# Performance work log

Measured on AMD Instinct MI355X. Metric: run time of the kernel, lower is better.

## Reference

```python
import jax, jax.numpy as jnp
import numpy as np

SEQ_LEN = 4096
EMBED = 1024
HIDDEN = 128
BATCH = 8


def setup_inputs() -> dict:
    key = jax.random.key(0)
    k_in, k_q, k_k, k_v = jax.random.split(key, 4)
    inputs = jax.random.normal(k_in, (BATCH, SEQ_LEN, EMBED), dtype=jnp.float32)
    # nn.Linear(embed, hidden, bias=False) weights; stored [hidden, embed] in torch,
    # we keep [embed, hidden] for x @ W.
    scale = 1.0 / np.sqrt(EMBED)
    Wq = jax.random.uniform(k_q, (EMBED, HIDDEN), jnp.float32, -scale, scale)
    Wk = jax.random.uniform(k_k, (EMBED, HIDDEN), jnp.float32, -scale, scale)
    Wv = jax.random.uniform(k_v, (EMBED, HIDDEN), jnp.float32, -scale, scale)
    return {"inputs": inputs, "Wq": Wq, "Wk": Wk, "Wv": Wv}


def reference(inputs, Wq, Wk, Wv):
    # Single-head causal scaled dot-product attention.
    q = jnp.einsum("bse,eh->bsh", inputs, Wq)
    k = jnp.einsum("bse,eh->bsh", inputs, Wk)
    v = jnp.einsum("bse,eh->bsh", inputs, Wv)
    d_k = q.shape[-1]
    q = q / jnp.sqrt(jnp.asarray(d_k, q.dtype))
    scores = jnp.einsum("bqh,bkh->bqk", q, k)  # [B, S, S]
    seq = scores.shape[-1]
    causal = jnp.tril(jnp.ones((seq, seq), dtype=bool))
    scores = jnp.where(causal, scores, jnp.asarray(-jnp.inf, scores.dtype))
    weights = jax.nn.softmax(scores, axis=-1)
    return jnp.einsum("bqk,bkh->bqh", weights, v)
```

## Files before the change

### kernel.cpp

```cpp
#include <hip/hip_runtime.h>
#include <stdint.h>

#define B_ 8
#define S_ 4096
#define E_ 1024
#define H_ 128
#define M_ (B_*S_)

typedef __attribute__((ext_vector_type(8))) short short8;
typedef __attribute__((ext_vector_type(4))) float f32x4;
typedef __attribute__((ext_vector_type(16))) float f32x16;

static constexpr float QSCALE = 0.08838834764831845f;

__device__ __forceinline__ unsigned short f2bf(float f) {
    uint32_t u = __float_as_uint(f);
    u += 0x7fffu + ((u >> 16) & 1u);
    return (unsigned short)(u >> 16);
}

__device__ __forceinline__ uint32_t cvt_pk_bf16(float a, float b) {
    uint32_t r;
    asm("v_cvt_pk_bf16_f32 %0, %1, %2" : "=v"(r) : "v"(a), "v"(b));
    return r;
}

__device__ __forceinline__ float bf2f(uint32_t u) {
    return __uint_as_float(u << 16);
}

__device__ __forceinline__ void gl16(const void* g, void* s) {
    __builtin_amdgcn_global_load_lds(
        (const __attribute__((address_space(1))) unsigned int*)g,
        (__attribute__((address_space(3))) unsigned int*)s, 16, 0, 0);
}

__global__ __launch_bounds__(256)
void prep_w_kernel(const float* __restrict__ Wq, const float* __restrict__ Wk,
                   const float* __restrict__ Wv, unsigned short* __restrict__ Wt)
{
    int id = blockIdx.x*256 + threadIdx.x;
    int which = id >> 14;
    int rem = id & 16383;
    int h = rem >> 7, kc = rem & 127;
    const float* __restrict__ W = (which==0)?Wq:((which==1)?Wk:Wv);
    const float scale = (which==0)? QSCALE : 1.0f;
    uint32_t u[4];
    #pragma unroll
    for (int p=0;p<4;++p) {
        unsigned short a = f2bf(W[(size_t)(kc*8 + 2*p  )*H_ + h] * scale);
        unsigned short b = f2bf(W[(size_t)(kc*8 + 2*p+1)*H_ + h] * scale);
        u[p] = (uint32_t)a | ((uint32_t)b << 16);
    }
    uint4 v; v.x=u[0]; v.y=u[1]; v.z=u[2]; v.w=u[3];
    int gp = (kc >> 3)*128 + (((kc & 7) ^ (h & 7)) << 4);
    *(uint4*)((unsigned char*)Wt + (size_t)(which*H_ + h)*2048 + gp) = v;
}

__device__ __forceinline__ void proj_stage(unsigned char* buf,
                                           const unsigned char* xb,
                                           const unsigned char* Wb,
                                           int i, int w, int l)
{
    #pragma unroll
    for (int j=0;j<8;++j) {
        int cb = (j*8 + w) * 1024;
        int A  = cb + (l << 4);
        if (cb < 16384) {
            int sub = A >> 13;
            int A2  = A & 8191;
            int row = A2 >> 7, col = A2 & 127;
            gl16(xb + (size_t)row*4096 + i*256 + sub*128 + (col ^ ((row & 7) << 4)),
                 buf + cb);
        } else {
            int A2 = A - 16384;
            int wr = A2 >> 7, wc = A2 & 127;
            gl16(Wb + (size_t)wr*2048 + i*128 + wc, buf + cb);
        }
    }
}

__global__ __launch_bounds__(512)
void proj_kernel(const float* __restrict__ x, const unsigned short* __restrict__ Wt,
                 unsigned short* __restrict__ Qg, unsigned short* __restrict__ Kg,
                 unsigned short* __restrict__ Vtg)
{
    const int t = threadIdx.x;
    const int w = t >> 6, l = t & 63;
    const int grp = l >> 4, li = l & 15;
    const int rg = w & 1, cg = w >> 1;
    const int rb = blockIdx.x;
    const int row0 = rb * 64;

    __shared__ __align__(128) unsigned char smem[65536];
    unsigned short* epi = (unsigned short*)smem;

    const unsigned char* xb = (const unsigned char*)x + (size_t)row0*4096;
    const unsigned char* Wb = (const unsigned char*)Wt;

    f32x4 acc[2][6];
    const f32x4 zz = {0.f,0.f,0.f,0.f};
    #pragma unroll
    for (int mt=0;mt<2;++mt)
        #pragma unroll
        for (int nt=0;nt<6;++nt) acc[mt][nt] = zz;

    proj_stage(smem, xb, Wb, 0, w, l);
    __syncthreads();

    for (int i=0; i<16; ++i) {
        const unsigned char* sX = smem;
        const unsigned char* sW = smem + 16384;

        #pragma unroll
        for (int ks=0;ks<2;++ks) {
            short8 af[2];
            #pragma unroll
            for (int mt=0;mt<2;++mt) {
                int row = rg*32 + mt*16 + li;
                int sw = (row & 7) << 4;
                float4 a0 = *(const float4*)(sX + ks*8192 + row*128 + ((grp*32     ) ^ sw));
                float4 a1 = *(const float4*)(sX + ks*8192 + row*128 + ((grp*32 + 16) ^ sw));
                union { uint32_t u[4]; short8 s; } pa;
                pa.u[0] = cvt_pk_bf16(a0.x, a0.y);
                pa.u[1] = cvt_pk_bf16(a0.z, a0.w);
                pa.u[2] = cvt_pk_bf16(a1.x, a1.y);
                pa.u[3] = cvt_pk_bf16(a1.z, a1.w);
                af[mt] = pa.s;
            }
            #pragma unroll
            for (int nt=0;nt<6;++nt) {
                int wr = cg*96 + nt*16 + li;
                short8 bf = *(const short8*)(sW + wr*128 + ((ks*64 + grp*16) ^ ((wr & 7) << 4)));
                acc[0][nt] = __builtin_amdgcn_mfma_f32_16x16x32_bf16(af[0], bf, acc[0][nt], 0,0,0);
                acc[1][nt] = __builtin_amdgcn_mfma_f32_16x16x32_bf16(af[1], bf, acc[1][nt], 0,0,0);
            }
        }

        __syncthreads();
        if (i+1 < 16) {
            proj_stage(smem, xb, Wb, i+1, w, l);
            __syncthreads();
        }
    }

    const int bidx = rb >> 6;
    const int srow = (rb & 63) * 64;

    if (cg < 2) {
        #pragma unroll
        for (int mt=0;mt<2;++mt)
            #pragma unroll
            for (int nt=0;nt<6;++nt)
                #pragma unroll
                for (int r=0;r<4;++r) {
                    int rowl = rg*32 + mt*16 + grp*4 + r;
                    int col  = cg*96 + nt*16 + li;
                    epi[rowl*208 + col] = f2bf(acc[mt][nt][r]);
                }
    }
    __syncthreads();
    #pragma unroll
    for (int i=0;i<2;++i) {
        int idx = i*512 + t;
        int row = idx >> 4, cc = idx & 15;
        uint4 v = *(const uint4*)((const unsigned char*)epi + row*416 + cc*16);
        *(uint4*)((unsigned char*)Qg + (size_t)(row0+row)*256 + cc*16) = v;
    }
    {
        int row = t >> 3, cc = t & 7;
        uint4 v = *(const uint4*)((const unsigned char*)epi + row*416 + 256 + cc*16);
        *(uint4*)((unsigned char*)Kg + (size_t)(row0+row)*256 + cc*16) = v;
    }
    __syncthreads();

    if (cg >= 2) {
        #pragma unroll
        for (int mt=0;mt<2;++mt)
            #pragma unroll
            for (int nt=0;nt<6;++nt)
                #pragma unroll
                for (int r=0;r<4;++r) {
                    int rowl = rg*32 + mt*16 + grp*4 + r;
                    int col  = (cg-2)*96 + nt*16 + li;
                    epi[rowl*208 + col] = f2bf(acc[mt][nt][r]);
                }
    }
    __syncthreads();
    {
        int row = t >> 3, cc = t & 7;
        uint4 v = *(const uint4*)((const unsigned char*)epi + row*416 + cc*16);
        *(uint4*)((unsigned char*)Kg + (size_t)(row0+row)*256 + 128 + cc*16) = v;
    }
    #pragma unroll
    for (int i=0;i<2;++i) {
        int idx = i*512 + t;
        int h = idx >> 3, sc = idx & 7;
        uint32_t u[4];
        #pragma unroll
        for (int p=0;p<4;++p) {
            unsigned short a = epi[(sc*8 + 2*p    )*208 + 64 + h];
            unsigned short b = epi[(sc*8 + 2*p + 1)*208 + 64 + h];
            u[p] = (uint32_t)a | ((uint32_t)b << 16);
        }
        uint4 v; v.x=u[0]; v.y=u[1]; v.z=u[2]; v.w=u[3];
        *(uint4*)(Vtg + (size_t)(bidx*H_ + h)*S_ + srow + sc*8) = v;
    }
}

__device__ __forceinline__ void stage_tile(unsigned char* buf,
                                           const unsigned char* Kb,
                                           const unsigned char* Vb,
                                           int kt, int w, int l)
{
    unsigned char* sVb = buf + 16384;
    #pragma unroll
    for (int j=0;j<2;++j) {
        int A = w*2048 + j*1024 + (l<<4);
        int krow = A >> 8;
        int kin  = A & 255;
        gl16(Kb + (size_t)kt*16384 + krow*256 + (kin ^ ((krow&7)<<4)),
             buf + w*2048 + j*1024);
        int h   = A >> 7;
        int vin = A & 127;
        gl16(Vb + (size_t)h*8192 + (size_t)kt*128 + (vin ^ ((h&7)<<4)),
             sVb + w*2048 + j*1024);
    }
}

__global__ __launch_bounds__(512, 2)
void attn_p1(const unsigned short* __restrict__ Qg,
             const unsigned short* __restrict__ Kg,
             const unsigned short* __restrict__ Vtg,
             unsigned short* __restrict__ Pp, float* __restrict__ Ml)
{
    const int t    = threadIdx.x;
    const int w    = t >> 6;
    const int l    = t & 63;
    const int hi   = l >> 5;
    const int c31  = l & 31;
    const int gid  = blockIdx.x;
    const int b    = gid & 7;
    const int rr   = gid >> 3;
    const int c4   = rr & 3;
    const int pr   = rr >> 2;

    __shared__ __align__(128) unsigned char smem[65536];

    const size_t bbase = (size_t)b * S_ * H_;
    const unsigned char* Kb = (const unsigned char*)(Kg + bbase);
    const unsigned char* Vb = (const unsigned char*)(Vtg + (size_t)b*H_*S_);
    const int swzq = (c31 & 7) << 4;

    int cur = 0;
    for (int ph = 0; ph < 2; ++ph) {
        const int qt   = ph ? (15 - pr) : pr;
        const int q0   = qt * 256;
        const int qw0  = q0 + w*32;
        const int qrow = qw0 + c31;
        const int nkt  = 4*(qt+1);

        short8 qf[8];
        {
            const unsigned short* qp = Qg + bbase + (size_t)qrow * H_;
            #pragma unroll
            for (int ks=0; ks<8; ++ks)
                qf[ks] = *(const short8*)(qp + ks*16 + hi*8);
        }

        f32x16 oacc[4];
        #pragma unroll
        for (int ht=0; ht<4; ++ht)
            #pragma unroll
            for (int r=0; r<16; ++r) oacc[ht][r] = 0.f;
        float mrun = -1e30f, lrun = 0.f;

        stage_tile(smem + cur*32768, Kb, Vb, c4, w, l);
        __syncthreads();

        for (int kt = c4; kt < nkt; kt += 4) {
            const bool pre = (kt+4 < nkt);
            if (pre) stage_tile(smem + (cur^1)*32768, Kb, Vb, kt+4, w, l);

            if (kt*64 <= qw0 + 31) {
                const unsigned char* sK = smem + cur*32768;
                const unsigned char* sV = sK + 16384;

                f32x16 sacc[2];
                #pragma unroll
                for (int st=0; st<2; ++st)
                    #pragma unroll
                    for (int r=0; r<16; ++r) sacc[st][r] = 0.f;
                #pragma unroll
                for (int st=0; st<2; ++st) {
                    int krow = st*32 + c31;
                    #pragma unroll
                    for (int ks=0; ks<8; ++ks) {
                        short8 kf = *(const short8*)(sK + krow*256 + ((ks*32 + hi*16) ^ swzq));
                        sacc[st] = __builtin_amdgcn_mfma_f32_32x32x16_bf16(kf, qf[ks], sacc[st], 0,0,0);
                    }
                }

                if (kt*64 + 63 > qw0) {
                    #pragma unroll
                    for (int st=0; st<2; ++st)
                        #pragma unroll
                        for (int r=0; r<16; ++r) {
                            int key = kt*64 + st*32 + (r&3) + 8*(r>>2) + 4*hi;
                            if (key > qrow) sacc[st][r] = -1e30f;
                        }
                }

                float pmax = -1e30f;
                #pragma unroll
                for (int st=0; st<2; ++st)
                    #pragma unroll
                    for (int r=0; r<16; ++r) pmax = fmaxf(pmax, sacc[st][r]);
                pmax = fmaxf(pmax, __shfl_xor(pmax, 32, 64));

                if (!__all(pmax - mrun <= 8.0f)) {
                    float mnew = fmaxf(mrun, pmax);
                    float alpha = __expf(mrun - mnew);
                    #pragma unroll
                    for (int ht=0; ht<4; ++ht)
                        #pragma unroll
                        for (int r=0; r<16; ++r) oacc[ht][r] *= alpha;
                    lrun *= alpha;
                    mrun = mnew;
                }

                float p[2][16];
                float psum = 0.f;
                #pragma unroll
                for (int st=0; st<2; ++st)
                    #pragma unroll
                    for (int r=0; r<16; ++r) {
                        float e = __expf(sacc[st][r] - mrun);
                        p[st][r] = e;
                        psum += e;
                    }
                psum += __shfl_xor(psum, 32, 64);
                lrun += psum;

                short8 pf[4];
                #pragma unroll
                for (int st=0; st<2; ++st) {
                    uint32_t A0 = cvt_pk_bf16(p[st][0],  p[st][1]);
                    uint32_t A1 = cvt_pk_bf16(p[st][2],  p[st][3]);
                    uint32_t B0 = cvt_pk_bf16(p[st][4],  p[st][5]);
                    uint32_t B1 = cvt_pk_bf16(p[st][6],  p[st][7]);
                    uint32_t C0 = cvt_pk_bf16(p[st][8],  p[st][9]);
                    uint32_t C1 = cvt_pk_bf16(p[st][10], p[st][11]);
                    uint32_t D0 = cvt_pk_bf16(p[st][12], p[st][13]);
                    uint32_t D1 = cvt_pk_bf16(p[st][14], p[st][15]);
                    {
                        uint32_t x0 = hi ? A0 : B0;
                        uint32_t x1 = hi ? A1 : B1;
                        uint32_t y0 = (uint32_t)__shfl_xor((int)x0, 32, 64);
                        uint32_t y1 = (uint32_t)__shfl_xor((int)x1, 32, 64);
                        union { uint32_t u[4]; short8 s; } uu;
                        uu.u[0] = hi ? y0 : A0;
                        uu.u[1] = hi ? y1 : A1;
                        uu.u[2] = hi ? B0 : y0;
                        uu.u[3] = hi ? B1 : y1;
                        pf[st*2] = uu.s;
                    }
                    {
                        uint32_t x0 = hi ? C0 : D0;
                        uint32_t x1 = hi ? C1 : D1;
                        uint32_t y0 = (uint32_t)__shfl_xor((int)x0, 32, 64);
                        uint32_t y1 = (uint32_t)__shfl_xor((int)x1, 32, 64);
                        union { uint32_t u[4]; short8 s; } uu;
                        uu.u[0] = hi ? y0 : C0;
                        uu.u[1] = hi ? y1 : C1;
                        uu.u[2] = hi ? D0 : y0;
                        uu.u[3] = hi ? D1 : y1;
                        pf[st*2+1] = uu.s;
                    }
                }

                #pragma unroll
                for (int sl=0; sl<4; ++sl) {
                    #pragma unroll
                    for (int ht=0; ht<4; ++ht) {
                        int h = ht*32 + c31;
                        short8 vf = *(const short8*)(sV + h*128 + ((sl*32 + hi*16) ^ swzq));
                        oacc[ht] = __builtin_amdgcn_mfma_f32_32x32x16_bf16(vf, pf[sl], oacc[ht], 0,0,0);
                    }
                }
            }

            __syncthreads();
            if (pre) cur ^= 1;
        }

        unsigned short* Prow = Pp + (size_t)c4*((size_t)M_*H_) + bbase + (size_t)qrow*H_;
        #pragma unroll
        for (int ht=0; ht<4; ++ht)
            #pragma unroll
            for (int k=0; k<4; ++k) {
                uint2 o;
                o.x = cvt_pk_bf16(oacc[ht][4*k+0], oacc[ht][4*k+1]);
                o.y = cvt_pk_bf16(oacc[ht][4*k+2], oacc[ht][4*k+3]);
                *(uint2*)(Prow + ht*32 + 8*k + 4*hi) = o;
            }
        if (hi == 0) {
            float2 ml2; ml2.x = mrun; ml2.y = lrun;
            *(float2*)(Ml + ((size_t)c4*M_ + (size_t)b*S_ + qrow)*2) = ml2;
        }
    }
}

__global__ __launch_bounds__(256)
void attn_merge(const unsigned short* __restrict__ Pp, const float* __restrict__ Ml,
                float* __restrict__ Out)
{
    int gid = blockIdx.x*256 + threadIdx.x;
    int q  = gid >> 5;
    int h4 = gid & 31;

    float m0 = Ml[((size_t)0*M_ + q)*2], l0 = Ml[((size_t)0*M_ + q)*2 + 1];
    float m1 = Ml[((size_t)1*M_ + q)*2], l1 = Ml[((size_t)1*M_ + q)*2 + 1];
    float m2 = Ml[((size_t)2*M_ + q)*2], l2 = Ml[((size_t)2*M_ + q)*2 + 1];
    float m3 = Ml[((size_t)3*M_ + q)*2], l3 = Ml[((size_t)3*M_ + q)*2 + 1];

    float M = fmaxf(fmaxf(m0, m1), fmaxf(m2, m3));
    float w0 = __expf(m0 - M), w1 = __expf(m1 - M);
    float w2 = __expf(m2 - M), w3 = __expf(m3 - M);
    float L = w0*l0 + w1*l1 + w2*l2 + w3*l3;

    uint2 u0 = *(const uint2*)(Pp + (size_t)0*((size_t)M_*H_) + (size_t)q*H_ + h4*4);
    uint2 u1 = *(const uint2*)(Pp + (size_t)1*((size_t)M_*H_) + (size_t)q*H_ + h4*4);
    uint2 u2 = *(const uint2*)(Pp + (size_t)2*((size_t)M_*H_) + (size_t)q*H_ + h4*4);
    uint2 u3 = *(const uint2*)(Pp + (size_t)3*((size_t)M_*H_) + (size_t)q*H_ + h4*4);
    float inv = 1.0f / L;
    float4 o;
    o.x = (w0*bf2f(u0.x & 0xffffu) + w1*bf2f(u1.x & 0xffffu)
         + w2*bf2f(u2.x & 0xffffu) + w3*bf2f(u3.x & 0xffffu)) * inv;
    o.y = (w0*bf2f(u0.x >> 16)     + w1*bf2f(u1.x >> 16)
         + w2*bf2f(u2.x >> 16)     + w3*bf2f(u3.x >> 16)) * inv;
    o.z = (w0*bf2f(u0.y & 0xffffu) + w1*bf2f(u1.y & 0xffffu)
         + w2*bf2f(u2.y & 0xffffu) + w3*bf2f(u3.y & 0xffffu)) * inv;
    o.w = (w0*bf2f(u0.y >> 16)     + w1*bf2f(u1.y >> 16)
         + w2*bf2f(u2.y >> 16)     + w3*bf2f(u3.y >> 16)) * inv;
    *(float4*)(Out + (size_t)q*H_ + h4*4) = o;
}

__global__ __launch_bounds__(128, 1)
void attn_fb(const unsigned short* __restrict__ Qg,
             const unsigned short* __restrict__ Kg,
             const unsigned short* __restrict__ Vtg,
             float* __restrict__ Out)
{
    const int t   = threadIdx.x;
    const int w   = t >> 6;
    const int l   = t & 63;
    const int hi  = l >> 5;
    const int c31 = l & 31;
    const int qt  = (S_/64 - 1) - blockIdx.x;
    const int b   = blockIdx.y;
    const int q0  = qt * 64;
    const int qrow = q0 + w*32 + c31;

    __shared__ __align__(128) unsigned char sK[16384];
    __shared__ __align__(128) unsigned char sV[16384];

    const size_t bbase = (size_t)b * S_ * H_;

    short8 qf[8];
    {
        const unsigned short* qp = Qg + bbase + (size_t)qrow * H_;
        #pragma unroll
        for (int ks=0; ks<8; ++ks)
            qf[ks] = *(const short8*)(qp + ks*16 + hi*8);
    }

    f32x16 oacc[4];
    #pragma unroll
    for (int ht=0; ht<4; ++ht)
        #pragma unroll
        for (int r=0; r<16; ++r) oacc[ht][r] = 0.f;
    float mrun = -1e30f, lrun = 0.f;

    const unsigned char* Kb = (const unsigned char*)(Kg + bbase);
    const unsigned char* Vb = (const unsigned char*)(Vtg + (size_t)b*H_*S_);
    const int swzq = (c31 & 7) << 4;

    for (int kt=0; kt<=qt; ++kt) {
        __syncthreads();
        #pragma unroll
        for (int i=0;i<8;++i) {
            int c = i*128 + t;
            int row = c >> 4, cb = (c & 15) * 16;
            *(uint4*)(sK + row*256 + (cb ^ ((row&7)<<4))) =
                *(const uint4*)(Kb + (size_t)(kt*64 + row)*256 + cb);
        }
        #pragma unroll
        for (int i=0;i<8;++i) {
            int c = i*128 + t;
            int h = c >> 3, cb = (c & 7) * 16;
            *(uint4*)(sV + h*128 + (cb ^ ((h&7)<<4))) =
                *(const uint4*)(Vb + (size_t)h*(S_*2) + kt*128 + cb);
        }
        __syncthreads();

        f32x16 sacc[2];
        #pragma unroll
        for (int st=0; st<2; ++st)
            #pragma unroll
            for (int r=0; r<16; ++r) sacc[st][r] = 0.f;
        #pragma unroll
        for (int st=0; st<2; ++st) {
            int krow = st*32 + c31;
            #pragma unroll
            for (int ks=0; ks<8; ++ks) {
                short8 kf = *(const short8*)(sK + krow*256 + ((ks*32 + hi*16) ^ swzq));
                sacc[st] = __builtin_amdgcn_mfma_f32_32x32x16_bf16(kf, qf[ks], sacc[st], 0,0,0);
            }
        }

        if (kt == qt) {
            #pragma unroll
            for (int st=0; st<2; ++st)
                #pragma unroll
                for (int r=0; r<16; ++r) {
                    int key = q0 + st*32 + (r&3) + 8*(r>>2) + 4*hi;
                    if (key > qrow) sacc[st][r] = -1e30f;
                }
        }

        float pmax = -1e30f;
        #pragma unroll
        for (int st=0; st<2; ++st)
            #pragma unroll
            for (int r=0; r<16; ++r) pmax = fmaxf(pmax, sacc[st][r]);
        pmax = fmaxf(pmax, __shfl_xor(pmax, 32, 64));

        if (!__all(pmax - mrun <= 8.0f)) {
            float mnew = fmaxf(mrun, pmax);
            float alpha = __expf(mrun - mnew);
            #pragma unroll
            for (int ht=0; ht<4; ++ht)
                #pragma unroll
                for (int r=0; r<16; ++r) oacc[ht][r] *= alpha;
            lrun *= alpha;
            mrun = mnew;
        }

        float p[2][16];
        float psum = 0.f;
        #pragma unroll
        for (int st=0; st<2; ++st)
            #pragma unroll
            for (int r=0; r<16; ++r) {
                float e = __expf(sacc[st][r] - mrun);
                p[st][r] = e;
                psum += e;
            }
        psum += __shfl_xor(psum, 32, 64);
        lrun += psum;

        short8 pf[4];
        #pragma unroll
        for (int st=0; st<2; ++st) {
            uint32_t A0 = cvt_pk_bf16(p[st][0],  p[st][1]);
            uint32_t A1 = cvt_pk_bf16(p[st][2],  p[st][3]);
            uint32_t B0 = cvt_pk_bf16(p[st][4],  p[st][5]);
            uint32_t B1 = cvt_pk_bf16(p[st][6],  p[st][7]);
            uint32_t C0 = cvt_pk_bf16(p[st][8],  p[st][9]);
            uint32_t C1 = cvt_pk_bf16(p[st][10], p[st][11]);
            uint32_t D0 = cvt_pk_bf16(p[st][12], p[st][13]);
            uint32_t D1 = cvt_pk_bf16(p[st][14], p[st][15]);
            {
                uint32_t x0 = hi ? A0 : B0;
                uint32_t x1 = hi ? A1 : B1;
                uint32_t y0 = (uint32_t)__shfl_xor((int)x0, 32, 64);
                uint32_t y1 = (uint32_t)__shfl_xor((int)x1, 32, 64);
                union { uint32_t u[4]; short8 s; } uu;
                uu.u[0] = hi ? y0 : A0;
                uu.u[1] = hi ? y1 : A1;
                uu.u[2] = hi ? B0 : y0;
                uu.u[3] = hi ? B1 : y1;
                pf[st*2] = uu.s;
            }
            {
                uint32_t x0 = hi ? C0 : D0;
                uint32_t x1 = hi ? C1 : D1;
                uint32_t y0 = (uint32_t)__shfl_xor((int)x0, 32, 64);
                uint32_t y1 = (uint32_t)__shfl_xor((int)x1, 32, 64);
                union { uint32_t u[4]; short8 s; } uu;
                uu.u[0] = hi ? y0 : C0;
                uu.u[1] = hi ? y1 : C1;
                uu.u[2] = hi ? D0 : y0;
                uu.u[3] = hi ? D1 : y1;
                pf[st*2+1] = uu.s;
            }
        }

        #pragma unroll
        for (int sl=0; sl<4; ++sl) {
            #pragma unroll
            for (int ht=0; ht<4; ++ht) {
                int h = ht*32 + c31;
                short8 vf = *(const short8*)(sV + h*128 + ((sl*32 + hi*16) ^ swzq));
                oacc[ht] = __builtin_amdgcn_mfma_f32_32x32x16_bf16(vf, pf[sl], oacc[ht], 0,0,0);
            }
        }
    }

    float linv = 1.0f / lrun;
    float* Op = Out + bbase + (size_t)qrow * H_;
    #pragma unroll
    for (int ht=0; ht<4; ++ht)
        #pragma unroll
        for (int k=0; k<4; ++k) {
            float4 o;
            o.x = oacc[ht][4*k+0] * linv;
            o.y = oacc[ht][4*k+1] * linv;
            o.z = oacc[ht][4*k+2] * linv;
            o.w = oacc[ht][4*k+3] * linv;
            *(float4*)(Op + ht*32 + 8*k + 4*hi) = o;
        }
}

extern "C" void kernel_launch(void* const* d_in, const int* in_sizes, int n_in,
                              void* d_out, int out_size, void* d_ws, size_t ws_size,
                              hipStream_t stream) {
    const float* x  = (const float*)d_in[0];
    const float* Wq = (const float*)d_in[1];
    const float* Wk = (const float*)d_in[2];
    const float* Wv = (const float*)d_in[3];

    unsigned char* ws = (unsigned char*)d_ws;
    unsigned short* Wt  = (unsigned short*)ws;
    unsigned short* Qg  = (unsigned short*)(ws + 1048576u);
    unsigned short* Kg  = (unsigned short*)(ws + 9437184u);
    unsigned short* Vtg = (unsigned short*)(ws + 17825792u);
    unsigned short* Pp  = (unsigned short*)(ws + 26214400u);
    float* Ml = (float*)(ws + 59768832u);
    const size_t NEED = 60817408u;

    prep_w_kernel<<<192, 256, 0, stream>>>(Wq, Wk, Wv, Wt);
    proj_kernel<<<512, 512, 0, stream>>>(x, Wt, Qg, Kg, Vtg);

    if (ws_size >= NEED) {
        attn_p1<<<256, 512, 0, stream>>>(Qg, Kg, Vtg, Pp, Ml);
        attn_merge<<<4096, 256, 0, stream>>>(Pp, Ml, (float*)d_out);
    } else {
        dim3 ga(S_/64, B_);
        attn_fb<<<ga, 128, 0, stream>>>(Qg, Kg, Vtg, (float*)d_out);
    }
}
```

Before: 105.4 us.

## Load projection operands directly from global memory instead of LDS staging

The QKV projection kernel no longer stages x and the transposed weights through a swizzled 64KB shared-memory buffer with barriers. Each lane now reads its MFMA fragments straight from global memory, with the weight prep writing a plain unswizzled layout. Shared memory shrinks to what the epilogue needs, which may raise occupancy and removes the synchronisation. In exchange, x rows and weights are re-read per wave through cache with less coalescing, and loads are no longer overlapped explicitly.

```diff
diff --git a/kernel.cpp b/kernel.cpp
--- a/kernel.cpp
+++ b/kernel.cpp
@@ -53,31 +53,7 @@
         u[p] = (uint32_t)a | ((uint32_t)b << 16);
     }
     uint4 v; v.x=u[0]; v.y=u[1]; v.z=u[2]; v.w=u[3];
-    int gp = (kc >> 3)*128 + (((kc & 7) ^ (h & 7)) << 4);
-    *(uint4*)((unsigned char*)Wt + (size_t)(which*H_ + h)*2048 + gp) = v;
-}
-
-__device__ __forceinline__ void proj_stage(unsigned char* buf,
-                                           const unsigned char* xb,
-                                           const unsigned char* Wb,
-                                           int i, int w, int l)
-{
-    #pragma unroll
-    for (int j=0;j<8;++j) {
-        int cb = (j*8 + w) * 1024;
-        int A  = cb + (l << 4);
-        if (cb < 16384) {
-            int sub = A >> 13;
-            int A2  = A & 8191;
-            int row = A2 >> 7, col = A2 & 127;
-            gl16(xb + (size_t)row*4096 + i*256 + sub*128 + (col ^ ((row & 7) << 4)),
-                 buf + cb);
-        } else {
-            int A2 = A - 16384;
-            int wr = A2 >> 7, wc = A2 & 127;
-            gl16(Wb + (size_t)wr*2048 + i*128 + wc, buf + cb);
-        }
-    }
+    *(uint4*)(Wt + (size_t)(which*H_ + h)*E_ + kc*8) = v;
 }
 
 __global__ __launch_bounds__(512)
@@ -92,11 +68,8 @@
     const int rb = blockIdx.x;
     const int row0 = rb * 64;
 
-    __shared__ __align__(128) unsigned char smem[65536];
+    __shared__ __align__(128) unsigned char smem[26624];
     unsigned short* epi = (unsigned short*)smem;
-
-    const unsigned char* xb = (const unsigned char*)x + (size_t)row0*4096;
-    const unsigned char* Wb = (const unsigned char*)Wt;
 
     f32x4 acc[2][6];
     const f32x4 zz = {0.f,0.f,0.f,0.f};
@@ -105,42 +78,39 @@
         #pragma unroll
         for (int nt=0;nt<6;++nt) acc[mt][nt] = zz;
 
-    proj_stage(smem, xb, Wb, 0, w, l);
-    __syncthreads();
-
-    for (int i=0; i<16; ++i) {
-        const unsigned char* sX = smem;
-        const unsigned char* sW = smem + 16384;
-
-        #pragma unroll
-        for (int ks=0;ks<2;++ks) {
-            short8 af[2];
-            #pragma unroll
-            for (int mt=0;mt<2;++mt) {
-                int row = rg*32 + mt*16 + li;
-                int sw = (row & 7) << 4;
-                float4 a0 = *(const float4*)(sX + ks*8192 + row*128 + ((grp*32     ) ^ sw));
-                float4 a1 = *(const float4*)(sX + ks*8192 + row*128 + ((grp*32 + 16) ^ sw));
-                union { uint32_t u[4]; short8 s; } pa;
-                pa.u[0] = cvt_pk_bf16(a0.x, a0.y);
-                pa.u[1] = cvt_pk_bf16(a0.z, a0.w);
-                pa.u[2] = cvt_pk_bf16(a1.x, a1.y);
-                pa.u[3] = cvt_pk_bf16(a1.z, a1.w);
-                af[mt] = pa.s;
-            }
-            #pragma unroll
-            for (int nt=0;nt<6;++nt) {
-                int wr = cg*96 + nt*16 + li;
-                short8 bf = *(const short8*)(sW + wr*128 + ((ks*64 + grp*16) ^ ((wr & 7) << 4)));
-                acc[0][nt] = __builtin_amdgcn_mfma_f32_16x16x32_bf16(af[0], bf, acc[0][nt], 0,0,0);
-                acc[1][nt] = __builtin_amdgcn_mfma_f32_16x16x32_bf16(af[1], bf, acc[1][nt], 0,0,0);
-            }
-        }
-
-        __syncthreads();
-        if (i+1 < 16) {
-            proj_stage(smem, xb, Wb, i+1, w, l);
-            __syncthreads();
+    const float* xr0 = x + (size_t)(row0 + rg*32      + li) * E_ + grp*8;
+    const float* xr1 = x + (size_t)(row0 + rg*32 + 16 + li) * E_ + grp*8;
+    const unsigned char* wbase = (const unsigned char*)Wt
+                               + (size_t)(cg*96 + li) * 2048 + grp*16;
+
+    #pragma unroll 4
+    for (int k0 = 0; k0 < E_; k0 += 32) {
+        short8 af[2];
+        {
+            float4 a0 = *(const float4*)(xr0 + k0);
+            float4 a1 = *(const float4*)(xr0 + k0 + 4);
+            union { uint32_t u[4]; short8 s; } pa;
+            pa.u[0] = cvt_pk_bf16(a0.x, a0.y);
+            pa.u[1] = cvt_pk_bf16(a0.z, a0.w);
+            pa.u[2] = cvt_pk_bf16(a1.x, a1.y);
+            pa.u[3] = cvt_pk_bf16(a1.z, a1.w);
+            af[0] = pa.s;
+        }
+        {
+            float4 a0 = *(const float4*)(xr1 + k0);
+            float4 a1 = *(const float4*)(xr1 + k0 + 4);
+            union { uint32_t u[4]; short8 s; } pa;
+            pa.u[0] = cvt_pk_bf16(a0.x, a0.y);
+            pa.u[1] = cvt_pk_bf16(a0.z, a0.w);
+            pa.u[2] = cvt_pk_bf16(a1.x, a1.y);
+            pa.u[3] = cvt_pk_bf16(a1.z, a1.w);
+            af[1] = pa.s;
+        }
+        #pragma unroll
+        for (int nt=0;nt<6;++nt) {
+            short8 bf = *(const short8*)(wbase + (size_t)nt*16*2048 + k0*2);
+            acc[0][nt] = __builtin_amdgcn_mfma_f32_16x16x32_bf16(af[0], bf, acc[0][nt], 0,0,0);
+            acc[1][nt] = __builtin_amdgcn_mfma_f32_16x16x32_bf16(af[1], bf, acc[1][nt], 0,0,0);
         }
     }
 
```

Result: slower. 211.8 us (+101.0%).
